# Optimization experiments

Hardware: AMD Instinct MI355X
Metric: run time of the kernel (lower is better)

Reference implementation:

```python
import jax, jax.numpy as jnp
import numpy as np

B, S, D, K = 16, 4096, 64, 4096

def setup_inputs() -> dict:
    key = jax.random.key(0)
    k1, k2 = jax.random.split(key)
    z = jax.random.normal(k1, (B, S, D), dtype=jnp.float32)
    # codebook initialized uniform(-1/K, 1/K) as in the torch module
    emb = jax.random.uniform(k2, (K, D), dtype=jnp.float32, minval=-1.0 / K, maxval=1.0 / K)
    return {"z": z, "emb": emb}

def reference(z, emb):
    Dm = emb.shape[1]
    flat_z = z.reshape(-1, Dm)                     # [N, D]
    # squared L2 distances to every codebook entry: [N, K]
    dist = (jnp.sum(flat_z * flat_z, axis=1, keepdims=True)
            + jnp.sum(emb * emb, axis=1)
            - 2.0 * flat_z @ emb.T)
    encoding_indices = jnp.argmin(dist, axis=1)    # [N]
    # one-hot @ emb is mathematically a gather; use the direct gather
    quantized = emb[encoding_indices].reshape(z.shape)
    quantized_st = z + jax.lax.stop_gradient(quantized - z)
    e_latent_loss = jnp.mean((jax.lax.stop_gradient(quantized) - z) ** 2)
    q_latent_loss = jnp.mean((quantized - jax.lax.stop_gradient(z)) ** 2)
    vq_loss = e_latent_loss + q_latent_loss
    return quantized_st, encoding_indices.reshape(z.shape[:-1]), vq_loss
```

## Files before the change

kernel.cpp:

```cpp
#include <hip/hip_runtime.h>

#define NTOK 65536
#define DDIM 64
#define KCB  4096
#define MB   64
#define NTILES 256
#define TPW  64
#define LCAP 4096
#define WWIN 5.0e-4f
#define IDXOFF  (NTOK * DDIM)
#define LOSSOFF (NTOK * DDIM + NTOK)
#define ZPAD 68

typedef __bf16 bf16x8 __attribute__((ext_vector_type(8)));
typedef float  f32x4  __attribute__((ext_vector_type(4)));

__device__ __forceinline__ float opaque(float x) { asm volatile("" : "+v"(x)); return x; }

__device__ __forceinline__ float np_sumsq64(const float* __restrict__ v) {
    float r[8];
#pragma unroll
    for (int j = 0; j < 8; ++j) r[j] = opaque(v[j] * v[j]);
#pragma unroll
    for (int i = 1; i < 8; ++i)
#pragma unroll
        for (int j = 0; j < 8; ++j) r[j] += opaque(v[8 * i + j] * v[8 * i + j]);
    return ((r[0] + r[1]) + (r[2] + r[3])) + ((r[4] + r[5]) + (r[6] + r[7]));
}

__device__ __forceinline__ unsigned short bf16rne(float x) {
    unsigned u = __float_as_uint(x);
    return (unsigned short)((u + 0x7fffu + ((u >> 16) & 1u)) >> 16);
}

__global__ void k_prep(const float* __restrict__ emb, float* __restrict__ e2,
                       uint4* __restrict__ pfh, double* __restrict__ lossacc) {
    int k = blockIdx.x * blockDim.x + threadIdx.x;
    if (k == 0) *lossacc = 0.0;
    if (k >= KCB) return;
    float row[DDIM];
    const float4* r4 = (const float4*)(emb + (size_t)k * DDIM);
#pragma unroll
    for (int i = 0; i < DDIM / 4; ++i) {
        float4 v = r4[i];
        row[4*i+0] = v.x; row[4*i+1] = v.y; row[4*i+2] = v.z; row[4*i+3] = v.w;
    }
    e2[k] = np_sumsq64(row);
    const int tile = k >> 4, rr = k & 15;
#pragma unroll
    for (int q = 0; q < 4; ++q) {
#pragma unroll
        for (int kh = 0; kh < 2; ++kh) {
            union { uint4 v; unsigned short s[8]; } th;
#pragma unroll
            for (int j = 0; j < 8; ++j) th.s[j] = bf16rne(row[q*8 + kh*32 + j]);
            pfh[(size_t)tile * 128 + kh * 64 + q * 16 + rr] = th.v;
        }
    }
}

__global__ __launch_bounds__(256, 4)
void k_vq(const float* __restrict__ z, const float* __restrict__ emb,
          const float* __restrict__ e2g, const uint4* __restrict__ pfh,
          float* __restrict__ out, double* __restrict__ lossacc) {
    __shared__ float z2s[MB];
    __shared__ unsigned v0u[MB];
    __shared__ unsigned long long keys[MB];
    __shared__ unsigned list[LCAP];
    __shared__ int lcnt;
    __shared__ float red[256];
    __shared__ int bidx_s[MB];
    __shared__ float zrow_s[MB][ZPAD];

    const int tid  = threadIdx.x;
    const int lane = tid & 63;
    const int l15  = lane & 15;
    const int quad = lane >> 4;
    const int wn   = tid >> 6;
    const int tok0 = blockIdx.x * MB;
    const size_t zbase = (size_t)tok0 * DDIM;

    if (tid < MB) { v0u[tid] = 0x7f800000u; keys[tid] = 0xFFFFFFFFFFFFFFFFull; }
    if (tid == 0) lcnt = 0;

    bf16x8 Ah[4][2];
#pragma unroll
    for (int ms = 0; ms < 4; ++ms) {
        const float* p = z + zbase + (size_t)(ms * 16 + l15) * DDIM + quad * 8;
#pragma unroll
        for (int kh = 0; kh < 2; ++kh) {
            float4 u0 = *(const float4*)(p + kh * 32);
            float4 u1 = *(const float4*)(p + kh * 32 + 4);
            float d[8] = {-(u0.x + u0.x), -(u0.y + u0.y), -(u0.z + u0.z), -(u0.w + u0.w),
                          -(u1.x + u1.x), -(u1.y + u1.y), -(u1.z + u1.z), -(u1.w + u1.w)};
            union { bf16x8 v; unsigned short u[8]; } th;
#pragma unroll
            for (int j = 0; j < 8; ++j) th.u[j] = bf16rne(d[j]);
            Ah[ms][kh] = th.v;
        }
    }

#pragma unroll
    for (int it = 0; it < 4; ++it) {
        int f = it * 256 + tid;
        int tt = f >> 4, cc = f & 15;
        float4 v = ((const float4*)(z + zbase))[f];
        *(float4*)&zrow_s[tt][cc * 4] = v;
    }
    __syncthreads();

    if (tid < MB) {
        float row[DDIM];
#pragma unroll
        for (int i = 0; i < DDIM / 4; ++i) {
            float4 v = *(const float4*)&zrow_s[tid][i * 4];
            row[4*i+0] = v.x; row[4*i+1] = v.y; row[4*i+2] = v.z; row[4*i+3] = v.w;
        }
        z2s[tid] = np_sumsq64(row);
    }

    float thr[16];
#pragma unroll
    for (int i = 0; i < 16; ++i) thr[i] = 3.0e38f;

    const uint4* pbase = pfh + (size_t)(wn * TPW) * 128 + lane;
    const int ncbase = (wn * TPW) * 16 + l15;

    auto commit_reload = [&]() {
#pragma unroll
        for (int i = 0; i < 16; ++i) {
            float v = thr[i] - WWIN;
            v = fminf(v, __shfl_xor(v, 1));
            v = fminf(v, __shfl_xor(v, 2));
            v = fminf(v, __shfl_xor(v, 4));
            v = fminf(v, __shfl_xor(v, 8));
            if (l15 == 0)
                atomicMin(&v0u[(i>>2)*16 + quad*4 + (i&3)], __float_as_uint(v));
        }
#pragma unroll
        for (int i = 0; i < 16; ++i) {
            float g = __uint_as_float(v0u[(i>>2)*16 + quad*4 + (i&3)]);
            thr[i] = fminf(thr[i], g + WWIN);
        }
    };

#pragma unroll 1
    for (int t = 0; t < 8; ++t) {
        union { uint4 q; bf16x8 v; } b0, b1;
        b0.q = pbase[(size_t)t * 128]; b1.q = pbase[(size_t)t * 128 + 64];
#pragma unroll
        for (int ms = 0; ms < 4; ++ms) {
            f32x4 a = {0.5f, 0.5f, 0.5f, 0.5f};
            a = __builtin_amdgcn_mfma_f32_16x16x32_bf16(Ah[ms][0], b0.v, a, 0, 0, 0);
            a = __builtin_amdgcn_mfma_f32_16x16x32_bf16(Ah[ms][1], b1.v, a, 0, 0, 0);
#pragma unroll
            for (int r = 0; r < 4; ++r)
                thr[ms*4+r] = fminf(thr[ms*4+r], a[r] + WWIN);
        }
    }
    commit_reload();

    auto compute2 = [&](uint4 p0, uint4 p1, uint4 q0, uint4 q1, int t) {
        unsigned mask = 0;
        {
            union { uint4 q; bf16x8 v; } b0, b1;
            b0.q = p0; b1.q = p1;
#pragma unroll
            for (int ms = 0; ms < 4; ++ms) {
                f32x4 a = {0.5f, 0.5f, 0.5f, 0.5f};
                a = __builtin_amdgcn_mfma_f32_16x16x32_bf16(Ah[ms][0], b0.v, a, 0, 0, 0);
                a = __builtin_amdgcn_mfma_f32_16x16x32_bf16(Ah[ms][1], b1.v, a, 0, 0, 0);
#pragma unroll
                for (int r = 0; r < 4; ++r) {
                    const int i = ms * 4 + r;
                    float h = a[r];
                    mask |= (h <= thr[i]) ? (1u << i) : 0u;
                    thr[i] = fminf(thr[i], h + WWIN);
                }
            }
        }
        {
            union { uint4 q; bf16x8 v; } b0, b1;
            b0.q = q0; b1.q = q1;
#pragma unroll
            for (int ms = 0; ms < 4; ++ms) {
                f32x4 a = {0.5f, 0.5f, 0.5f, 0.5f};
                a = __builtin_amdgcn_mfma_f32_16x16x32_bf16(Ah[ms][0], b0.v, a, 0, 0, 0);
                a = __builtin_amdgcn_mfma_f32_16x16x32_bf16(Ah[ms][1], b1.v, a, 0, 0, 0);
#pragma unroll
                for (int r = 0; r < 4; ++r) {
                    const int i = ms * 4 + r;
                    float h = a[r];
                    mask |= (h <= thr[i]) ? (1u << (16 + i)) : 0u;
                    thr[i] = fminf(thr[i], h + WWIN);
                }
            }
        }
        if (__ballot(mask != 0)) {
            while (mask) {
                int b = __builtin_ctz(mask);
                mask &= mask - 1;
                int ts = b >> 4, i = b & 15;
                int m = (i >> 2) * 16 + quad * 4 + (i & 3);
                int ncol = ncbase + (t + ts) * 16;
                int idx = atomicAdd(&lcnt, 1);
                if (idx < LCAP)
                    list[idx] = ((unsigned)m << 12) | (unsigned)ncol;
            }
        }
    };

    uint4 a0 = pbase[0],   a1 = pbase[64];
    uint4 b0 = pbase[128], b1 = pbase[192];
    const uint4* pf = pbase + 256;
#pragma unroll 1
    for (int t = 0; t < TPW; t += 2) {
        uint4 c0 = a0, c1 = a1, d0 = b0, d1 = b1;
        if (t + 2 < TPW) {
            c0 = pf[0]; c1 = pf[64]; d0 = pf[128]; d1 = pf[192];
            pf += 256;
        }
        compute2(a0, a1, b0, b1, t);
        a0 = c0; a1 = c1; b0 = d0; b1 = d1;
        if ((t & 7) == 6 && t + 2 < TPW) commit_reload();
    }
    __syncthreads();

    int cnt = lcnt; if (cnt > LCAP) cnt = LCAP;
    for (int i = tid; i < cnt; i += 256) {
        unsigned e = list[i];
        int m = (int)(e >> 12), n = (int)(e & 4095u);
        const float4* er4 = (const float4*)(emb + (size_t)n * DDIM);
        const float4* zr4 = (const float4*)&zrow_s[m][0];
        float a = 0.f;
#pragma unroll
        for (int j4 = 0; j4 < 16; ++j4) {
            float4 ev = er4[j4];
            float4 zv = zr4[j4];
            a = fmaf(zv.x + zv.x, ev.x, a);
            a = fmaf(zv.y + zv.y, ev.y, a);
            a = fmaf(zv.z + zv.z, ev.z, a);
            a = fmaf(zv.w + zv.w, ev.w, a);
        }
        float s = (z2s[m] + e2g[n]) - a;
        unsigned long long key = ((unsigned long long)__float_as_uint(s) << 32)
                               | (unsigned long long)(unsigned)n;
        atomicMin(&keys[m], key);
    }
    __syncthreads();

    if (tid < MB) {
        int nstar = (int)(keys[tid] & 0xffffffffULL);
        bidx_s[tid] = nstar;
        out[IDXOFF + tok0 + tid] = (float)nstar;
    }
    __syncthreads();

    float lsum = 0.f;
#pragma unroll
    for (int it = 0; it < 4; ++it) {
        int f  = it * 256 + tid;
        int tt = f >> 4, cc = f & 15;
        int idx = bidx_s[tt];
        float4 qv = ((const float4*)(emb + (size_t)idx * DDIM))[cc];
        float4 zv = *(const float4*)&zrow_s[tt][cc * 4];
        ((float4*)(out + zbase))[f] = qv;
        float dx = qv.x - zv.x, dy = qv.y - zv.y;
        float dz = qv.z - zv.z, dw = qv.w - zv.w;
        lsum += dx * dx + dy * dy + dz * dz + dw * dw;
    }
    red[tid] = lsum;
    __syncthreads();
    for (int s = 128; s > 0; s >>= 1) {
        if (tid < s) red[tid] += red[tid + s];
        __syncthreads();
    }
    if (tid == 0) atomicAdd(lossacc, (double)red[0]);
}

__global__ void k_fin(const double* __restrict__ lossacc, float* __restrict__ out) {
    out[LOSSOFF] = (float)(2.0 * (*lossacc) / (double)(NTOK * DDIM));
}

extern "C" void kernel_launch(void* const* d_in, const int* in_sizes, int n_in,
                              void* d_out, int out_size, void* d_ws, size_t ws_size,
                              hipStream_t stream) {
    const float* z   = (const float*)d_in[0];
    const float* emb = (const float*)d_in[1];
    float* out = (float*)d_out;

    char* ws = (char*)d_ws;
    float*  e2g     = (float*)(ws);
    uint4*  pfh     = (uint4*)(ws + 16384);
    double* lossacc = (double*)(ws + 16384 + 524288);

    hipLaunchKernelGGL(k_prep, dim3(64), dim3(64), 0, stream, emb, e2g, pfh, lossacc);
    hipLaunchKernelGGL(k_vq, dim3(NTOK / MB), dim3(256), 0, stream,
                       z, emb, e2g, pfh, out, lossacc);
    hipLaunchKernelGGL(k_fin, dim3(1), dim3(1), 0, stream, lossacc, out);
}
```

Baseline: 171.5 us.

## Use a fixed block-wide pruning threshold from a prescan instead of an adaptive one

The candidate-pruning threshold used to be a running per-lane minimum, refined every few tiles by shuffles and shared atomics. It is now computed once: each wave prescans its first 8 codebook tiles, the block reduces those minima with one barrier, and that fixed threshold gates every later tile. This removes the per-element threshold updates, the periodic commit/reload rounds and the ballot branch from the hot MFMA loop. In exchange the threshold is looser, so more candidates may be exactly rescored. The candidate list grows to 6144 entries, and the loss-reduction buffer reuses the list's shared memory, but the larger list can still overflow and raises LDS use, which may lower occupancy.

```diff
diff --git a/kernel.cpp b/kernel.cpp
--- a/kernel.cpp
+++ b/kernel.cpp
@@ -6,7 +6,7 @@
 #define MB   64
 #define NTILES 256
 #define TPW  64
-#define LCAP 4096
+#define LCAP 6144
 #define WWIN 5.0e-4f
 #define IDXOFF  (NTOK * DDIM)
 #define LOSSOFF (NTOK * DDIM + NTOK)
@@ -68,7 +68,6 @@
     __shared__ unsigned long long keys[MB];
     __shared__ unsigned list[LCAP];
     __shared__ int lcnt;
-    __shared__ float red[256];
     __shared__ int bidx_s[MB];
     __shared__ float zrow_s[MB][ZPAD];
 
@@ -119,31 +118,12 @@
         z2s[tid] = np_sumsq64(row);
     }
 
-    float thr[16];
-#pragma unroll
-    for (int i = 0; i < 16; ++i) thr[i] = 3.0e38f;
-
     const uint4* pbase = pfh + (size_t)(wn * TPW) * 128 + lane;
     const int ncbase = (wn * TPW) * 16 + l15;
 
-    auto commit_reload = [&]() {
-#pragma unroll
-        for (int i = 0; i < 16; ++i) {
-            float v = thr[i] - WWIN;
-            v = fminf(v, __shfl_xor(v, 1));
-            v = fminf(v, __shfl_xor(v, 2));
-            v = fminf(v, __shfl_xor(v, 4));
-            v = fminf(v, __shfl_xor(v, 8));
-            if (l15 == 0)
-                atomicMin(&v0u[(i>>2)*16 + quad*4 + (i&3)], __float_as_uint(v));
-        }
-#pragma unroll
-        for (int i = 0; i < 16; ++i) {
-            float g = __uint_as_float(v0u[(i>>2)*16 + quad*4 + (i&3)]);
-            thr[i] = fminf(thr[i], g + WWIN);
-        }
-    };
-
+    float rm[16];
+#pragma unroll
+    for (int i = 0; i < 16; ++i) rm[i] = 3.0e38f;
 #pragma unroll 1
     for (int t = 0; t < 8; ++t) {
         union { uint4 q; bf16x8 v; } b0, b1;
@@ -154,11 +134,25 @@
             a = __builtin_amdgcn_mfma_f32_16x16x32_bf16(Ah[ms][0], b0.v, a, 0, 0, 0);
             a = __builtin_amdgcn_mfma_f32_16x16x32_bf16(Ah[ms][1], b1.v, a, 0, 0, 0);
 #pragma unroll
-            for (int r = 0; r < 4; ++r)
-                thr[ms*4+r] = fminf(thr[ms*4+r], a[r] + WWIN);
-        }
-    }
-    commit_reload();
+            for (int r = 0; r < 4; ++r) rm[ms*4+r] = fminf(rm[ms*4+r], a[r]);
+        }
+    }
+#pragma unroll
+    for (int i = 0; i < 16; ++i) {
+        float v = rm[i];
+        v = fminf(v, __shfl_xor(v, 1));
+        v = fminf(v, __shfl_xor(v, 2));
+        v = fminf(v, __shfl_xor(v, 4));
+        v = fminf(v, __shfl_xor(v, 8));
+        if (l15 == 0)
+            atomicMin(&v0u[(i >> 2) * 16 + quad * 4 + (i & 3)], __float_as_uint(v));
+    }
+    __syncthreads();
+
+    float thr[16];
+#pragma unroll
+    for (int i = 0; i < 16; ++i)
+        thr[i] = __uint_as_float(v0u[(i >> 2) * 16 + quad * 4 + (i & 3)]) + WWIN;
 
     auto compute2 = [&](uint4 p0, uint4 p1, uint4 q0, uint4 q1, int t) {
         unsigned mask = 0;
@@ -173,9 +167,7 @@
 #pragma unroll
                 for (int r = 0; r < 4; ++r) {
                     const int i = ms * 4 + r;
-                    float h = a[r];
-                    mask |= (h <= thr[i]) ? (1u << i) : 0u;
-                    thr[i] = fminf(thr[i], h + WWIN);
+                    mask |= (a[r] <= thr[i]) ? (1u << i) : 0u;
                 }
             }
         }
@@ -190,23 +182,19 @@
 #pragma unroll
                 for (int r = 0; r < 4; ++r) {
                     const int i = ms * 4 + r;
-                    float h = a[r];
-                    mask |= (h <= thr[i]) ? (1u << (16 + i)) : 0u;
-                    thr[i] = fminf(thr[i], h + WWIN);
+                    mask |= (a[r] <= thr[i]) ? (1u << (16 + i)) : 0u;
                 }
             }
         }
-        if (__ballot(mask != 0)) {
-            while (mask) {
-                int b = __builtin_ctz(mask);
-                mask &= mask - 1;
-                int ts = b >> 4, i = b & 15;
-                int m = (i >> 2) * 16 + quad * 4 + (i & 3);
-                int ncol = ncbase + (t + ts) * 16;
-                int idx = atomicAdd(&lcnt, 1);
-                if (idx < LCAP)
-                    list[idx] = ((unsigned)m << 12) | (unsigned)ncol;
-            }
+        while (mask) {
+            int b = __builtin_ctz(mask);
+            mask &= mask - 1;
+            int ts = b >> 4, i = b & 15;
+            int m = (i >> 2) * 16 + quad * 4 + (i & 3);
+            int ncol = ncbase + (t + ts) * 16;
+            int idx = atomicAdd(&lcnt, 1);
+            if (idx < LCAP)
+                list[idx] = ((unsigned)m << 12) | (unsigned)ncol;
         }
     };
 
@@ -222,7 +210,6 @@
         }
         compute2(a0, a1, b0, b1, t);
         a0 = c0; a1 = c1; b0 = d0; b1 = d1;
-        if ((t & 7) == 6 && t + 2 < TPW) commit_reload();
     }
     __syncthreads();
 
@@ -256,6 +243,7 @@
     }
     __syncthreads();
 
+    float* red = (float*)list;
     float lsum = 0.f;
 #pragma unroll
     for (int it = 0; it < 4; ++it) {
```

Result: no change. 168.7 us (-1.6%).
